# Optimization experiments

Measured on AMD Instinct MI355X. Metric: run time of the kernel, lower is better.

Reference implementation:

```python
import jax, jax.numpy as jnp
import numpy as np

B, D, H, W = 2, 16, 16, 16
N = D * H * W
CDESC = 64
TEMP = 0.07
TOPK = 24
RADIUS = 0.45


def flatten_spatial(x):
    # (B, C, D, H, W) -> (B, N, C)
    b, c = x.shape[:2]
    return x.reshape(b, c, -1).transpose(0, 2, 1)


def voxel_grid():
    # normalized voxel-center grid in [-1, 1], shape (3, D, H, W)
    zs = jnp.linspace(-1.0, 1.0, D)
    ys = jnp.linspace(-1.0, 1.0, H)
    xs = jnp.linspace(-1.0, 1.0, W)
    return jnp.stack(jnp.meshgrid(zs, ys, xs, indexing='ij'), axis=0)


def setup_inputs() -> dict:
    key = jax.random.key(0)
    ks = jax.random.split(key, 8)
    return {
        'src_canonical': jax.random.normal(ks[0], (B, 3, D, H, W), jnp.float32),
        'tgt_canonical': jax.random.normal(ks[1], (B, 3, D, H, W), jnp.float32),
        'src_desc': jax.random.normal(ks[2], (B, CDESC, D, H, W), jnp.float32),
        'tgt_desc': jax.random.normal(ks[3], (B, CDESC, D, H, W), jnp.float32),
        'src_mlogits': jax.random.normal(ks[4], (B, 2, D, H, W), jnp.float32),
        'tgt_mlogits': jax.random.normal(ks[5], (B, 2, D, H, W), jnp.float32),
        'src_unc': jax.random.uniform(ks[6], (B, 1, D, H, W), jnp.float32),
        'tgt_unc': jax.random.uniform(ks[7], (B, 1, D, H, W), jnp.float32),
    }


def reference(src_canonical, tgt_canonical, src_desc, tgt_desc,
              src_mlogits, tgt_mlogits, src_unc, tgt_unc):
    sc = flatten_spatial(src_canonical)  # (B, N, 3)
    tc = flatten_spatial(tgt_canonical)  # (B, N, 3)
    sd = flatten_spatial(src_desc)       # (B, N, C)
    td = flatten_spatial(tgt_desc)       # (B, N, C)

    # torch.cdist: Euclidean distance matrix (B, N, N)
    d2 = (jnp.sum(sc * sc, -1)[:, :, None]
          + jnp.sum(tc * tc, -1)[:, None, :]
          - 2.0 * jnp.einsum('bid,bjd->bij', sc, tc))
    dist = jnp.sqrt(jnp.maximum(d2, 1e-12))

    sim = jnp.einsum('bid,bjd->bij', sd, td)  # (B, N, N)

    k = min(TOPK, N)
    _, nn_idx = jax.lax.top_k(-dist, k)  # k smallest distances per row
    bidx = jnp.arange(B)[:, None, None]
    ridx = jnp.arange(N)[None, :, None]
    allowed = jnp.zeros((B, N, N), bool).at[bidx, ridx, nn_idx].set(True)
    allowed = allowed | (dist <= RADIUS)

    tgt_match = jax.nn.softmax(flatten_spatial(tgt_mlogits), axis=-1)[..., 0]  # (B, N)
    src_match = jax.nn.softmax(flatten_spatial(src_mlogits), axis=-1)[..., 0]  # (B, N)

    # (B, N, 1) + (B, 1, N) rank-1 uncertainty penalty
    unc = flatten_spatial(src_unc) + flatten_spatial(tgt_unc).transpose(0, 2, 1)

    scores = sim - dist - 0.1 * unc
    scores = jnp.where(allowed, scores, -10000.0)
    # legacy matchability score mode
    scores = scores + jnp.maximum(jnp.log(tgt_match), -20.0)[:, None, :]
    probs = jax.nn.softmax(scores / TEMP, axis=-1)
    probs = jnp.nan_to_num(probs, nan=0.0, posinf=0.0, neginf=0.0)

    tpos = voxel_grid().reshape(3, -1).T  # (N, 3)
    expected = jnp.einsum('bij,jd->bid', probs, tpos)  # (B, N, 3)
    src_pos = jnp.broadcast_to(tpos, (B, N, 3))

    disp = (expected - src_pos).transpose(0, 2, 1).reshape(B, 3, D, H, W)
    disp = jnp.nan_to_num(disp, nan=0.0, posinf=0.0, neginf=0.0)

    conf = (jnp.max(probs, axis=-1) * src_match).reshape(B, 1, D, H, W)

    ent = -jnp.sum(probs * jnp.log(jnp.clip(probs, 1e-12, None)), axis=-1)
    ent = jnp.nan_to_num(ent, nan=0.0, posinf=0.0, neginf=0.0).reshape(B, 1, D, H, W)

    return expected, disp, probs, conf, ent, src_pos
```

## Files before the change

kernel.cpp:

```cpp
#include <hip/hip_runtime.h>
#include <math.h>
#include <stddef.h>

#define NN    4096
#define BATCH 2
#define CD    64
#define KSEL  24
#define RAD2  0.2025f
#define NBINS 256
#define KBASE 1888
#define LCAP  255
#define CCAP  64
#define NCP   4

typedef float f4v __attribute__((ext_vector_type(4)));

__device__ __forceinline__ int d2key(unsigned bits) {
  int k = (int)(bits >> 19) - KBASE;
  return k < 0 ? 0 : (k > NBINS - 1 ? NBINS - 1 : k);
}

__device__ __forceinline__ int wave_bin24(const int (*h)[NBINS], int lane, int* cb_out) {
  int4 a = ((const int4*)h[0])[lane];
  int4 b = ((const int4*)h[1])[lane];
  int4 c = ((const int4*)h[2])[lane];
  int4 d = ((const int4*)h[3])[lane];
  int tt[4] = {a.x + b.x + c.x + d.x, a.y + b.y + c.y + d.y,
               a.z + b.z + c.z + d.z, a.w + b.w + c.w + d.w};
  int s = tt[0] + tt[1] + tt[2] + tt[3];
  int inc = s;
#pragma unroll
  for (int off = 1; off < 64; off <<= 1) {
    int t = __shfl_up(inc, off);
    if (lane >= off) inc += t;
  }
  int below = inc - s;
  int Bl = -1, Bb = 0;
#pragma unroll
  for (int q = 0; q < 4; ++q) {
    if (Bl < 0 && below < KSEL && below + tt[q] >= KSEL) { Bl = 4 * lane + q; Bb = below; }
    below += tt[q];
  }
  unsigned long long mk = __ballot(Bl >= 0);
  if (!mk) return -1;
  int sl = __ffsll((long long)mk) - 1;
  *cb_out = __shfl(Bb, sl);
  return __shfl(Bl, sl);
}

__global__ __launch_bounds__(256)
void prep_all(const float* __restrict__ td, const float* __restrict__ sd,
              const float* __restrict__ tml, const float* __restrict__ tu,
              float* __restrict__ tdT, float* __restrict__ sdT,
              float* __restrict__ addj) {
  __shared__ float tile[64][65];
  int blk = blockIdx.x;
  if (blk < 256) {
    const float* src = (blk < 128) ? td  : sd;
    float*       dst = (blk < 128) ? tdT : sdT;
    int lb = blk & 127;
    int b  = lb >> 6;
    int j0 = (lb & 63) << 6;
    int jl = threadIdx.x & 63;
    int cq = threadIdx.x >> 6;
    const float* srcp = src + (size_t)b * CD * NN;
#pragma unroll
    for (int r = 0; r < 16; ++r) {
      int c = r * 4 + cq;
      tile[c][jl] = srcp[(size_t)c * NN + j0 + jl];
    }
    __syncthreads();
    float* dstp = dst + (size_t)b * NN * CD;
#pragma unroll
    for (int r = 0; r < 16; ++r) {
      int j = r * 4 + cq;
      dstp[(size_t)(j0 + j) * CD + jl] = tile[jl][j];
    }
  } else {
    int idx = (blk - 256) * 256 + threadIdx.x;
    if (idx < BATCH * NN) {
      int b = idx >> 12, j = idx & (NN - 1);
      float l0 = tml[(size_t)b * 2 * NN + j];
      float l1 = tml[(size_t)b * 2 * NN + NN + j];
      float x  = l1 - l0;
      float sp = fmaxf(x, 0.0f) + log1pf(expf(-fabsf(x)));
      addj[idx] = fmaxf(-sp, -20.0f) - 0.1f * tu[idx];
    }
  }
}

__global__ __launch_bounds__(256, 8)
void matcher_main(const float* __restrict__ sc, const float* __restrict__ tc,
                  const float* __restrict__ sd, const float* __restrict__ td,
                  const float* __restrict__ tdT, const float* __restrict__ sdT,
                  const float* __restrict__ addj,
                  const float* __restrict__ tml, const float* __restrict__ tu,
                  const float* __restrict__ sml,
                  float* __restrict__ oexp, float* __restrict__ odisp,
                  float* __restrict__ oprob, float* __restrict__ oconf,
                  float* __restrict__ oent, float* __restrict__ osrc) {
  __shared__ __align__(16) unsigned idxb[NN / 4];
  __shared__ __align__(16) int      hist[NCP][NBINS];
  __shared__ __align__(16) float4   sdp4[CD / 4];
  __shared__ int2     lst[LCAP];
  __shared__ int2     slist[256];
  __shared__ unsigned cand[CCAP];
  __shared__ int      lcount, candn;

  const int tid  = threadIdx.x;
  const int w    = tid >> 6;
  const int lane = tid & 63;
  const int row  = blockIdx.x;
  const int b    = row >> 12;
  const int i    = row & (NN - 1);
  const unsigned RADB = __float_as_uint(RAD2);

  ((int4*)hist)[tid] = make_int4(0, 0, 0, 0);
#pragma unroll
  for (int q = 0; q < 4; ++q) idxb[(q << 8) + tid] = 0u;
  if (sdT) { if (tid < 16) sdp4[tid] = ((const float4*)(sdT + ((size_t)b * NN + i) * CD))[tid]; }
  else     { if (tid < 64) ((float*)sdp4)[tid] = sd[(size_t)b * CD * NN + (size_t)tid * NN + i]; }
  if (tid == 0) { lcount = 0; candn = 0; }

  const float* scb = sc + (size_t)b * 3 * NN;
  const float s0 = scb[i], s1 = scb[NN + i], s2 = scb[2 * NN + i];
  const float4* tcx = (const float4*)(tc + (size_t)b * 3 * NN);
  const float4* tcy = tcx + NN / 4;
  const float4* tcz = tcy + NN / 4;
  __syncthreads();

  unsigned d2b[16];
#pragma unroll
  for (int k = 0; k < 4; ++k) {
    int g = (k << 8) + tid;
    float4 X = tcx[g], Y = tcy[g], Z = tcz[g];
    float xs[4] = {X.x, X.y, X.z, X.w};
    float ys[4] = {Y.x, Y.y, Y.z, Y.w};
    float zs[4] = {Z.x, Z.y, Z.z, Z.w};
#pragma unroll
    for (int r = 0; r < 4; ++r) {
      float dx = xs[r] - s0, dy = ys[r] - s1, dz = zs[r] - s2;
      float d2 = fmaxf(__fmaf_rn(dx, dx, __fmaf_rn(dy, dy, dz * dz)), 1e-12f);
      unsigned bits = __float_as_uint(d2);
      d2b[(k << 2) + r] = bits;
      if (d2 < 2.0f) atomicAdd(&hist[w][d2key(bits)], 1);
    }
  }
  __syncthreads();

  int cb = 0;
  int Bs = wave_bin24(hist, lane, &cb);
  if (Bs < 0) {
    __syncthreads();
#pragma unroll
    for (int m = 0; m < 16; ++m)
      if (__uint_as_float(d2b[m]) >= 2.0f) atomicAdd(&hist[w][d2key(d2b[m])], 1);
    __syncthreads();
    Bs = wave_bin24(hist, lane, &cb);
  }

  {
    int wtot = 0;
#pragma unroll
    for (int m = 0; m < 16; ++m) {
      unsigned bits = d2b[m];
      bool p = (d2key(bits) <= Bs) | (bits <= RADB);
      unsigned long long mk = __ballot(p);
      wtot += (int)__popcll(mk);
    }
    int wbase = 0;
    if (lane == 0) wbase = atomicAdd(&lcount, wtot);
    wbase = __shfl(wbase, 0);
    const unsigned long long lmask = (1ull << lane) - 1ull;
    int run = wbase;
#pragma unroll
    for (int m = 0; m < 16; ++m) {
      unsigned bits = d2b[m];
      int key = d2key(bits);
      bool p = (key <= Bs) | (bits <= RADB);
      unsigned long long mk = __ballot(p);
      if (p) {
        int idx = run + (int)__popcll(mk & lmask);
        if (idx < LCAP) {
          int j = ((m >> 2) << 10) + (tid << 2) + (m & 3);
          ((unsigned char*)idxb)[j] = (unsigned char)(idx + 1);
          lst[idx] = make_int2(j, (int)bits);
        }
        if (key == Bs) {
          int c = atomicAdd(&candn, 1);
          if (c < CCAP) cand[c] = bits;
        }
      }
      run += (int)__popcll(mk);
    }
  }
  __syncthreads();
  const int na = lcount < LCAP ? lcount : LCAP;

  unsigned thrb;
  {
    int found = 0; unsigned fv = 0;
    const int Krem = KSEL - cb;
    if (candn <= CCAP) {
      int nc = candn;
      if (lane < nc) {
        unsigned v = cand[lane];
        int lt = 0, le = 0;
        for (int m = 0; m < nc; ++m) { unsigned u = cand[m]; lt += (u < v); le += (u <= v); }
        if (lt < Krem && le >= Krem) { found = 1; fv = v; }
      }
    } else {
      for (int e = lane; e < na; e += 64) {
        unsigned v = (unsigned)lst[e].y;
        int lt = 0, le = 0;
        for (int m = 0; m < na; ++m) {
          unsigned u = (unsigned)lst[m].y;
          lt += (u < v); le += (u <= v);
        }
        if (lt < KSEL && le >= KSEL) { found = 1; fv = v; }
      }
    }
    unsigned long long mk = __ballot(found != 0);
    unsigned d24 = (unsigned)__shfl((int)fv, __ffsll((long long)mk) - 1);
    thrb = d24 > RADB ? d24 : RADB;
  }

  const float* tdb = tdT ? tdT + (size_t)b * NN * CD : nullptr;
  if (tid < na) {
    int2 en = lst[tid];
    int j = en.x;
    unsigned bits = (unsigned)en.y;
    float d2 = __uint_as_float(bits);
    float a0 = 0.f, a1 = 0.f, a2 = 0.f, a3 = 0.f;
    if (tdb) {
      const float4* trow = (const float4*)(tdb + (size_t)j * CD);
#pragma unroll
      for (int q = 0; q < CD / 4; q += 4) {
        float4 x0 = sdp4[q],     t0 = trow[q];
        float4 x1 = sdp4[q + 1], t1 = trow[q + 1];
        float4 x2 = sdp4[q + 2], t2 = trow[q + 2];
        float4 x3 = sdp4[q + 3], t3 = trow[q + 3];
        a0 = fmaf(x0.x, t0.x, fmaf(x0.y, t0.y, fmaf(x0.z, t0.z, fmaf(x0.w, t0.w, a0))));
        a1 = fmaf(x1.x, t1.x, fmaf(x1.y, t1.y, fmaf(x1.z, t1.z, fmaf(x1.w, t1.w, a1))));
        a2 = fmaf(x2.x, t2.x, fmaf(x2.y, t2.y, fmaf(x2.z, t2.z, fmaf(x2.w, t2.w, a2))));
        a3 = fmaf(x3.x, t3.x, fmaf(x3.y, t3.y, fmaf(x3.z, t3.z, fmaf(x3.w, t3.w, a3))));
      }
    } else {
      const float* spx = (const float*)sdp4;
      const float* tp  = td + (size_t)b * CD * NN + j;
#pragma unroll 8
      for (int c2 = 0; c2 < CD; ++c2) a0 = fmaf(spx[c2], tp[(size_t)c2 * NN], a0);
    }
    float sim = (a0 + a1) + (a2 + a3);
    float aj;
    if (addj) {
      aj = addj[(size_t)b * NN + j];
    } else {
      float l0 = tml[(size_t)b * 2 * NN + j];
      float l1 = tml[(size_t)b * 2 * NN + NN + j];
      float x  = l1 - l0;
      float sp = fmaxf(x, 0.0f) + log1pf(expf(-fabsf(x)));
      aj = fmaxf(-sp, -20.0f) - 0.1f * tu[(size_t)b * NN + j];
    }
    float sco = (bits <= thrb) ? (sim - sqrtf(d2) + aj) : -1e30f;
    slist[tid] = make_int2(j, __float_as_int(sco));
  }
  __syncthreads();

  const float C1   = (1.0f / 0.07f) * 1.44269504089f;
  const float STEP = 2.0f / 15.0f;
  const float LN2  = 0.69314718056f;
  float m_ = -1e30f;
  for (int e = lane; e < na; e += 64) m_ = fmaxf(m_, __int_as_float(slist[e].y));
#pragma unroll
  for (int off = 32; off; off >>= 1) m_ = fmaxf(m_, __shfl_xor(m_, off));
  float zl = 0.f, eu = 0.f, e0 = 0.f, e1 = 0.f, e2 = 0.f;
  for (int e = lane; e < na; e += 64) {
    int2 sv = slist[e];
    float u  = (__int_as_float(sv.y) - m_) * C1;
    float ev = exp2f(u);
    int j = sv.x;
    float pz = -1.0f + STEP * (float)(j >> 8);
    float py = -1.0f + STEP * (float)((j >> 4) & 15);
    float px = -1.0f + STEP * (float)(j & 15);
    zl += ev; eu = fmaf(ev, u, eu);
    e0 = fmaf(ev, pz, e0); e1 = fmaf(ev, py, e1); e2 = fmaf(ev, px, e2);
  }
#pragma unroll
  for (int off = 32; off; off >>= 1) {
    zl += __shfl_xor(zl, off); eu += __shfl_xor(eu, off);
    e0 += __shfl_xor(e0, off); e1 += __shfl_xor(e1, off); e2 += __shfl_xor(e2, off);
  }
  const float invZ = 1.0f / zl;

  f4v* prow4 = (f4v*)(oprob + (size_t)row * NN);
#pragma unroll
  for (int q = 0; q < 4; ++q) {
    int c = (q << 8) + tid;
    unsigned pk = idxb[c];
    f4v v; v[0] = 0.f; v[1] = 0.f; v[2] = 0.f; v[3] = 0.f;
    if (pk) {
#pragma unroll
      for (int r = 0; r < 4; ++r) {
        unsigned u8 = (pk >> (8 * r)) & 0xFFu;
        if (u8) v[r] = exp2f((__int_as_float(slist[u8 - 1].y) - m_) * C1) * invZ;
      }
    }
    __builtin_nontemporal_store(v, &prow4[c]);
  }

  if (tid == 0) {
    float p0 = e0 * invZ, p1 = e1 * invZ, p2 = e2 * invZ;
    float ent = LN2 * (log2f(zl) - eu * invZ);
    float tz = -1.0f + STEP * (float)(i >> 8);
    float ty = -1.0f + STEP * (float)((i >> 4) & 15);
    float tx = -1.0f + STEP * (float)(i & 15);
    size_t r3 = (size_t)row * 3;
    oexp[r3 + 0] = p0; oexp[r3 + 1] = p1; oexp[r3 + 2] = p2;
    osrc[r3 + 0] = tz; osrc[r3 + 1] = ty; osrc[r3 + 2] = tx;
    size_t db = (size_t)b * 3 * NN;
    odisp[db + 0 * NN + i] = p0 - tz;
    odisp[db + 1 * NN + i] = p1 - ty;
    odisp[db + 2 * NN + i] = p2 - tx;
    float ls0 = sml[(size_t)b * 2 * NN + i];
    float ls1 = sml[(size_t)b * 2 * NN + NN + i];
    float smv = 1.0f / (1.0f + expf(ls1 - ls0));
    oconf[(size_t)b * NN + i] = invZ * smv;
    oent[(size_t)b * NN + i]  = ent;
  }
}

extern "C" void kernel_launch(void* const* d_in, const int* in_sizes, int n_in,
                              void* d_out, int out_size, void* d_ws, size_t ws_size,
                              hipStream_t stream) {
  const float* sc  = (const float*)d_in[0];
  const float* tc  = (const float*)d_in[1];
  const float* sd  = (const float*)d_in[2];
  const float* td  = (const float*)d_in[3];
  const float* sml = (const float*)d_in[4];
  const float* tml = (const float*)d_in[5];
  const float* tu  = (const float*)d_in[7];

  float* out   = (float*)d_out;
  float* oexp  = out;
  float* odisp = oexp  + (size_t)BATCH * NN * 3;
  float* oprob = odisp + (size_t)BATCH * NN * 3;
  float* oconf = oprob + (size_t)BATCH * NN * NN;
  float* oent  = oconf + (size_t)BATCH * NN;
  float* osrc  = oent  + (size_t)BATCH * NN;

  size_t need = ((size_t)2 * BATCH * NN * CD + (size_t)BATCH * NN) * sizeof(float);
  float* tdT = nullptr; float* sdT = nullptr; float* adj = nullptr;
  if (ws_size >= need) {
    tdT = (float*)d_ws;
    sdT = tdT + (size_t)BATCH * NN * CD;
    adj = sdT + (size_t)BATCH * NN * CD;
    prep_all<<<256 + 32, 256, 0, stream>>>(td, sd, tml, tu, tdT, sdT, adj);
  }
  matcher_main<<<BATCH * NN, 256, 0, stream>>>(sc, tc, sd, td, tdT, sdT, adj,
                                               tml, tu, sml,
                                               oexp, odisp, oprob, oconf, oent, osrc);
}
```

Baseline: 205.0 us.

## Compute allowed-neighbor scores wave-cooperatively in registers, skipping histogram when radius suffices

Drops the shared candidate list and byte index map. It first counts neighbors within the radius and runs the histogram top-k threshold search only when fewer than K fall inside it, with a bisection fallback. Each allowed neighbor's descriptor dot product is now computed by a whole wave (one channel per lane plus a shuffle reduction) instead of one thread per candidate. The softmax weights are kept in the per-thread distance registers so the probability row can be written without shared-memory lookups. In exchange, the scoring loop runs twice (once for the max, once for the sums), each allowed neighbor costs a serial wave iteration with reductions, and the 0.1 uncertainty term for the source voxel still seems to be missing from the score.

```diff
diff --git a/kernel.cpp b/kernel.cpp
--- a/kernel.cpp
+++ b/kernel.cpp
@@ -9,7 +9,6 @@
 #define RAD2  0.2025f
 #define NBINS 256
 #define KBASE 1888
-#define LCAP  255
 #define CCAP  64
 #define NCP   4
 
@@ -99,13 +98,11 @@
                   float* __restrict__ oexp, float* __restrict__ odisp,
                   float* __restrict__ oprob, float* __restrict__ oconf,
                   float* __restrict__ oent, float* __restrict__ osrc) {
-  __shared__ __align__(16) unsigned idxb[NN / 4];
-  __shared__ __align__(16) int      hist[NCP][NBINS];
-  __shared__ __align__(16) float4   sdp4[CD / 4];
-  __shared__ int2     lst[LCAP];
-  __shared__ int2     slist[256];
+  __shared__ __align__(16) int hist[NCP][NBINS];
   __shared__ unsigned cand[CCAP];
-  __shared__ int      lcount, candn;
+  __shared__ float red[4][8];
+  __shared__ int   ired[8];
+  __shared__ int   candn;
 
   const int tid  = threadIdx.x;
   const int w    = tid >> 6;
@@ -115,21 +112,16 @@
   const int i    = row & (NN - 1);
   const unsigned RADB = __float_as_uint(RAD2);
 
-  ((int4*)hist)[tid] = make_int4(0, 0, 0, 0);
-#pragma unroll
-  for (int q = 0; q < 4; ++q) idxb[(q << 8) + tid] = 0u;
-  if (sdT) { if (tid < 16) sdp4[tid] = ((const float4*)(sdT + ((size_t)b * NN + i) * CD))[tid]; }
-  else     { if (tid < 64) ((float*)sdp4)[tid] = sd[(size_t)b * CD * NN + (size_t)tid * NN + i]; }
-  if (tid == 0) { lcount = 0; candn = 0; }
-
   const float* scb = sc + (size_t)b * 3 * NN;
   const float s0 = scb[i], s1 = scb[NN + i], s2 = scb[2 * NN + i];
+  const float sdreg = sdT ? sdT[((size_t)b * NN + i) * CD + lane]
+                          : sd[(size_t)b * CD * NN + (size_t)lane * NN + i];
   const float4* tcx = (const float4*)(tc + (size_t)b * 3 * NN);
   const float4* tcy = tcx + NN / 4;
   const float4* tcz = tcy + NN / 4;
-  __syncthreads();
 
   unsigned d2b[16];
+  int crad = 0;
 #pragma unroll
   for (int k = 0; k < 4; ++k) {
     int g = (k << 8) + tid;
@@ -143,175 +135,173 @@
       float d2 = fmaxf(__fmaf_rn(dx, dx, __fmaf_rn(dy, dy, dz * dz)), 1e-12f);
       unsigned bits = __float_as_uint(d2);
       d2b[(k << 2) + r] = bits;
-      if (d2 < 2.0f) atomicAdd(&hist[w][d2key(bits)], 1);
-    }
-  }
+      crad += (bits <= RADB);
+    }
+  }
+#pragma unroll
+  for (int off = 32; off; off >>= 1) crad += __shfl_xor(crad, off);
+  if (lane == 0) ired[w] = crad;
   __syncthreads();
-
-  int cb = 0;
-  int Bs = wave_bin24(hist, lane, &cb);
-  if (Bs < 0) {
+  crad = ired[0] + ired[1] + ired[2] + ired[3];
+
+  unsigned thrb = RADB;
+  if (crad < KSEL) {
+    ((int4*)hist)[tid] = make_int4(0, 0, 0, 0);
+    if (tid == 0) candn = 0;
     __syncthreads();
-#pragma unroll
-    for (int m = 0; m < 16; ++m)
-      if (__uint_as_float(d2b[m]) >= 2.0f) atomicAdd(&hist[w][d2key(d2b[m])], 1);
-    __syncthreads();
-    Bs = wave_bin24(hist, lane, &cb);
-  }
-
-  {
-    int wtot = 0;
 #pragma unroll
     for (int m = 0; m < 16; ++m) {
       unsigned bits = d2b[m];
-      bool p = (d2key(bits) <= Bs) | (bits <= RADB);
-      unsigned long long mk = __ballot(p);
-      wtot += (int)__popcll(mk);
-    }
-    int wbase = 0;
-    if (lane == 0) wbase = atomicAdd(&lcount, wtot);
-    wbase = __shfl(wbase, 0);
-    const unsigned long long lmask = (1ull << lane) - 1ull;
-    int run = wbase;
+      if (__uint_as_float(bits) < 2.0f) atomicAdd(&hist[w][d2key(bits)], 1);
+    }
+    __syncthreads();
+    int cb = 0;
+    int Bs = wave_bin24(hist, lane, &cb);
+    if (Bs < 0) {
+      __syncthreads();
+#pragma unroll
+      for (int m = 0; m < 16; ++m)
+        if (__uint_as_float(d2b[m]) >= 2.0f) atomicAdd(&hist[w][d2key(d2b[m])], 1);
+      __syncthreads();
+      Bs = wave_bin24(hist, lane, &cb);
+    }
 #pragma unroll
     for (int m = 0; m < 16; ++m) {
-      unsigned bits = d2b[m];
-      int key = d2key(bits);
-      bool p = (key <= Bs) | (bits <= RADB);
-      unsigned long long mk = __ballot(p);
-      if (p) {
-        int idx = run + (int)__popcll(mk & lmask);
-        if (idx < LCAP) {
-          int j = ((m >> 2) << 10) + (tid << 2) + (m & 3);
-          ((unsigned char*)idxb)[j] = (unsigned char)(idx + 1);
-          lst[idx] = make_int2(j, (int)bits);
-        }
-        if (key == Bs) {
-          int c = atomicAdd(&candn, 1);
-          if (c < CCAP) cand[c] = bits;
-        }
-      }
-      run += (int)__popcll(mk);
-    }
-  }
-  __syncthreads();
-  const int na = lcount < LCAP ? lcount : LCAP;
-
-  unsigned thrb;
-  {
-    int found = 0; unsigned fv = 0;
+      if (d2key(d2b[m]) == Bs) { int c = atomicAdd(&candn, 1); if (c < CCAP) cand[c] = d2b[m]; }
+    }
+    __syncthreads();
+    unsigned d24;
     const int Krem = KSEL - cb;
     if (candn <= CCAP) {
       int nc = candn;
+      int found = 0; unsigned fv = 0;
       if (lane < nc) {
         unsigned v = cand[lane];
         int lt = 0, le = 0;
         for (int m = 0; m < nc; ++m) { unsigned u = cand[m]; lt += (u < v); le += (u <= v); }
         if (lt < Krem && le >= Krem) { found = 1; fv = v; }
       }
+      unsigned long long mk = __ballot(found != 0);
+      d24 = (unsigned)__shfl((int)fv, __ffsll((long long)mk) - 1);
     } else {
-      for (int e = lane; e < na; e += 64) {
-        unsigned v = (unsigned)lst[e].y;
-        int lt = 0, le = 0;
-        for (int m = 0; m < na; ++m) {
-          unsigned u = (unsigned)lst[m].y;
-          lt += (u < v); le += (u <= v);
-        }
-        if (lt < KSEL && le >= KSEL) { found = 1; fv = v; }
+      unsigned lo = (unsigned)(Bs + KBASE) << 19;
+      unsigned hi = (unsigned)(Bs + KBASE + 1) << 19;
+      while (lo + 1u < hi) {
+        unsigned mid = (lo + hi) >> 1;
+        int c = 0;
+#pragma unroll
+        for (int m = 0; m < 16; ++m) c += (d2b[m] <= mid);
+#pragma unroll
+        for (int off = 32; off; off >>= 1) c += __shfl_xor(c, off);
+        if (lane == 0) ired[4 + w] = c;
+        __syncthreads();
+        c = ired[4] + ired[5] + ired[6] + ired[7];
+        __syncthreads();
+        if (c >= KSEL) hi = mid; else lo = mid;
       }
-    }
-    unsigned long long mk = __ballot(found != 0);
-    unsigned d24 = (unsigned)__shfl((int)fv, __ffsll((long long)mk) - 1);
+      d24 = hi;
+    }
     thrb = d24 > RADB ? d24 : RADB;
   }
 
   const float* tdb = tdT ? tdT + (size_t)b * NN * CD : nullptr;
-  if (tid < na) {
-    int2 en = lst[tid];
-    int j = en.x;
-    unsigned bits = (unsigned)en.y;
-    float d2 = __uint_as_float(bits);
-    float a0 = 0.f, a1 = 0.f, a2 = 0.f, a3 = 0.f;
-    if (tdb) {
-      const float4* trow = (const float4*)(tdb + (size_t)j * CD);
-#pragma unroll
-      for (int q = 0; q < CD / 4; q += 4) {
-        float4 x0 = sdp4[q],     t0 = trow[q];
-        float4 x1 = sdp4[q + 1], t1 = trow[q + 1];
-        float4 x2 = sdp4[q + 2], t2 = trow[q + 2];
-        float4 x3 = sdp4[q + 3], t3 = trow[q + 3];
-        a0 = fmaf(x0.x, t0.x, fmaf(x0.y, t0.y, fmaf(x0.z, t0.z, fmaf(x0.w, t0.w, a0))));
-        a1 = fmaf(x1.x, t1.x, fmaf(x1.y, t1.y, fmaf(x1.z, t1.z, fmaf(x1.w, t1.w, a1))));
-        a2 = fmaf(x2.x, t2.x, fmaf(x2.y, t2.y, fmaf(x2.z, t2.z, fmaf(x2.w, t2.w, a2))));
-        a3 = fmaf(x3.x, t3.x, fmaf(x3.y, t3.y, fmaf(x3.z, t3.z, fmaf(x3.w, t3.w, a3))));
-      }
-    } else {
-      const float* spx = (const float*)sdp4;
-      const float* tp  = td + (size_t)b * CD * NN + j;
-#pragma unroll 8
-      for (int c2 = 0; c2 < CD; ++c2) a0 = fmaf(spx[c2], tp[(size_t)c2 * NN], a0);
-    }
-    float sim = (a0 + a1) + (a2 + a3);
-    float aj;
-    if (addj) {
-      aj = addj[(size_t)b * NN + j];
-    } else {
-      float l0 = tml[(size_t)b * 2 * NN + j];
-      float l1 = tml[(size_t)b * 2 * NN + NN + j];
-      float x  = l1 - l0;
-      float sp = fmaxf(x, 0.0f) + log1pf(expf(-fabsf(x)));
-      aj = fmaxf(-sp, -20.0f) - 0.1f * tu[(size_t)b * NN + j];
-    }
-    float sco = (bits <= thrb) ? (sim - sqrtf(d2) + aj) : -1e30f;
-    slist[tid] = make_int2(j, __float_as_int(sco));
-  }
-  __syncthreads();
-
   const float C1   = (1.0f / 0.07f) * 1.44269504089f;
   const float STEP = 2.0f / 15.0f;
   const float LN2  = 0.69314718056f;
-  float m_ = -1e30f;
-  for (int e = lane; e < na; e += 64) m_ = fmaxf(m_, __int_as_float(slist[e].y));
-#pragma unroll
-  for (int off = 32; off; off >>= 1) m_ = fmaxf(m_, __shfl_xor(m_, off));
+
+  float mloc = -1e30f;
+#pragma unroll 1
+  for (int m = 0; m < 16; ++m) {
+    unsigned long long mk = __ballot(d2b[m] <= thrb);
+    const int k = m >> 2, r = m & 3;
+    while (mk) {
+      int src = __ffsll((long long)mk) - 1;
+      mk &= mk - 1;
+      int j = (((k << 8) + (w << 6) + src) << 2) + r;
+      float tv = tdb ? tdb[(size_t)j * CD + lane]
+                     : td[(size_t)b * CD * NN + (size_t)lane * NN + j];
+      float part = sdreg * tv;
+#pragma unroll
+      for (int off = 32; off; off >>= 1) part += __shfl_xor(part, off);
+      unsigned bits = (unsigned)__shfl((int)d2b[m], src);
+      float aj;
+      if (addj) {
+        aj = addj[(size_t)b * NN + j];
+      } else {
+        float l0 = tml[(size_t)b * 2 * NN + j];
+        float l1 = tml[(size_t)b * 2 * NN + NN + j];
+        float x  = l1 - l0;
+        float sp = fmaxf(x, 0.0f) + log1pf(expf(-fabsf(x)));
+        aj = fmaxf(-sp, -20.0f) - 0.1f * tu[(size_t)b * NN + j];
+      }
+      float sco = part - sqrtf(__uint_as_float(bits)) + aj;
+      mloc = fmaxf(mloc, sco);
+    }
+  }
+  if (lane == 0) red[w][5] = mloc;
+  __syncthreads();
+  const float m_ = fmaxf(fmaxf(red[0][5], red[1][5]), fmaxf(red[2][5], red[3][5]));
+
   float zl = 0.f, eu = 0.f, e0 = 0.f, e1 = 0.f, e2 = 0.f;
-  for (int e = lane; e < na; e += 64) {
-    int2 sv = slist[e];
-    float u  = (__int_as_float(sv.y) - m_) * C1;
-    float ev = exp2f(u);
-    int j = sv.x;
-    float pz = -1.0f + STEP * (float)(j >> 8);
-    float py = -1.0f + STEP * (float)((j >> 4) & 15);
-    float px = -1.0f + STEP * (float)(j & 15);
-    zl += ev; eu = fmaf(ev, u, eu);
-    e0 = fmaf(ev, pz, e0); e1 = fmaf(ev, py, e1); e2 = fmaf(ev, px, e2);
-  }
-#pragma unroll
-  for (int off = 32; off; off >>= 1) {
-    zl += __shfl_xor(zl, off); eu += __shfl_xor(eu, off);
-    e0 += __shfl_xor(e0, off); e1 += __shfl_xor(e1, off); e2 += __shfl_xor(e2, off);
-  }
-  const float invZ = 1.0f / zl;
+#pragma unroll 1
+  for (int m = 0; m < 16; ++m) {
+    unsigned mybits = d2b[m];
+    bool p = (mybits <= thrb);
+    d2b[m] = 0u;
+    unsigned long long mk = __ballot(p);
+    const int k = m >> 2, r = m & 3;
+    while (mk) {
+      int src = __ffsll((long long)mk) - 1;
+      mk &= mk - 1;
+      int j = (((k << 8) + (w << 6) + src) << 2) + r;
+      float tv = tdb ? tdb[(size_t)j * CD + lane]
+                     : td[(size_t)b * CD * NN + (size_t)lane * NN + j];
+      float part = sdreg * tv;
+#pragma unroll
+      for (int off = 32; off; off >>= 1) part += __shfl_xor(part, off);
+      unsigned bits = (unsigned)__shfl((int)mybits, src);
+      float aj;
+      if (addj) {
+        aj = addj[(size_t)b * NN + j];
+      } else {
+        float l0 = tml[(size_t)b * 2 * NN + j];
+        float l1 = tml[(size_t)b * 2 * NN + NN + j];
+        float x  = l1 - l0;
+        float sp = fmaxf(x, 0.0f) + log1pf(expf(-fabsf(x)));
+        aj = fmaxf(-sp, -20.0f) - 0.1f * tu[(size_t)b * NN + j];
+      }
+      float sco = part - sqrtf(__uint_as_float(bits)) + aj;
+      float u   = (sco - m_) * C1;
+      float ev  = exp2f(u);
+      if (lane == src) d2b[m] = __float_as_uint(ev);
+      float pz = -1.0f + STEP * (float)(j >> 8);
+      float py = -1.0f + STEP * (float)((j >> 4) & 15);
+      float px = -1.0f + STEP * (float)(j & 15);
+      zl += ev; eu = fmaf(ev, u, eu);
+      e0 = fmaf(ev, pz, e0); e1 = fmaf(ev, py, e1); e2 = fmaf(ev, px, e2);
+    }
+  }
+  if (lane == 0) { red[w][0] = zl; red[w][1] = eu; red[w][2] = e0; red[w][3] = e1; red[w][4] = e2; }
+  __syncthreads();
+  const float Zt  = red[0][0] + red[1][0] + red[2][0] + red[3][0];
+  const float invZ = 1.0f / Zt;
 
   f4v* prow4 = (f4v*)(oprob + (size_t)row * NN);
 #pragma unroll
-  for (int q = 0; q < 4; ++q) {
-    int c = (q << 8) + tid;
-    unsigned pk = idxb[c];
-    f4v v; v[0] = 0.f; v[1] = 0.f; v[2] = 0.f; v[3] = 0.f;
-    if (pk) {
-#pragma unroll
-      for (int r = 0; r < 4; ++r) {
-        unsigned u8 = (pk >> (8 * r)) & 0xFFu;
-        if (u8) v[r] = exp2f((__int_as_float(slist[u8 - 1].y) - m_) * C1) * invZ;
-      }
-    }
-    __builtin_nontemporal_store(v, &prow4[c]);
+  for (int k = 0; k < 4; ++k) {
+    f4v v;
+#pragma unroll
+    for (int r = 0; r < 4; ++r) v[r] = __uint_as_float(d2b[(k << 2) + r]) * invZ;
+    __builtin_nontemporal_store(v, &prow4[(k << 8) + tid]);
   }
 
   if (tid == 0) {
-    float p0 = e0 * invZ, p1 = e1 * invZ, p2 = e2 * invZ;
-    float ent = LN2 * (log2f(zl) - eu * invZ);
+    float eut = red[0][1] + red[1][1] + red[2][1] + red[3][1];
+    float e0t = red[0][2] + red[1][2] + red[2][2] + red[3][2];
+    float e1t = red[0][3] + red[1][3] + red[2][3] + red[3][3];
+    float e2t = red[0][4] + red[1][4] + red[2][4] + red[3][4];
+    float p0 = e0t * invZ, p1 = e1t * invZ, p2 = e2t * invZ;
+    float ent = LN2 * (log2f(Zt) - eut * invZ);
     float tz = -1.0f + STEP * (float)(i >> 8);
     float ty = -1.0f + STEP * (float)((i >> 4) & 15);
     float tx = -1.0f + STEP * (float)(i & 15);
```

Result: slower. 274.5 us (+33.9%).
